# Optimization experiments

Hardware: AMD Instinct MI355X
Metric: run time of the kernel (lower is better)

Reference implementation:

```python
import jax, jax.numpy as jnp
import numpy as np

N = 100000   # total nodes (batched molecular graph)
E = 200000   # total edges
G = 5000     # number of graphs
NF = 16      # num_node_features
EF = 8       # num_edge_features
LD = 64      # latent_dim
EPS = 1e-5   # batch-norm eps (PyG BatchNorm default)


def setup_inputs() -> dict:
    key = jax.random.key(0)
    ks = jax.random.split(key, 20)
    s = 0.1  # weight scale
    return {
        'x': jax.random.normal(ks[0], (N, NF), dtype=jnp.float32),
        'edge_index': jax.random.randint(ks[1], (2, E), 0, N, dtype=jnp.int32),
        'edge_attr': jax.random.normal(ks[2], (E, EF), dtype=jnp.float32),
        'batch': jnp.sort(jax.random.randint(ks[3], (N,), 0, G, dtype=jnp.int32)),
        # ECC layer 1 (in=16 -> out=32)
        'We1': jax.random.normal(ks[4], (NF * 32, EF), dtype=jnp.float32) * s,
        'b1': jnp.zeros((32,), dtype=jnp.float32),
        'Wr1': jax.random.normal(ks[5], (32, NF), dtype=jnp.float32) * s,
        'g1': jnp.ones((32,), dtype=jnp.float32),
        'be1': jnp.zeros((32,), dtype=jnp.float32),
        # ECC layer 2 (in=32 -> out=64)
        'We2': jax.random.normal(ks[6], (32 * 64, EF), dtype=jnp.float32) * s,
        'b2': jnp.zeros((64,), dtype=jnp.float32),
        'Wr2': jax.random.normal(ks[7], (64, 32), dtype=jnp.float32) * s,
        'g2': jnp.ones((64,), dtype=jnp.float32),
        'be2': jnp.zeros((64,), dtype=jnp.float32),
        # dense tail
        'Wf1': jax.random.normal(ks[8], (128, 64), dtype=jnp.float32) * s,
        'bf1': jnp.zeros((128,), dtype=jnp.float32),
        'Wf2': jax.random.normal(ks[9], (2 * LD, 128), dtype=jnp.float32) * s,
        'bf2': jnp.zeros((2 * LD,), dtype=jnp.float32),
    }


def _ecc(x, src, dst, edge_attr, We, b, Wr, out_c):
    # theta: per-edge [out_c, in_c] filter matrices from edge features
    in_c = x.shape[1]
    theta = (edge_attr @ We.T).reshape(-1, out_c, in_c)       # [E, out, in]
    deg = jnp.zeros((x.shape[0],), x.dtype).at[src].add(1.0)   # degree over edge_index[0]
    norm = jnp.where(deg > 0, 1.0 / deg, 0.0)                  # [N]
    msg = jnp.einsum('eoi,ei->eo', theta, x[src]) * norm[src, None]  # [E, out]
    agg = jnp.zeros((x.shape[0], out_c), x.dtype).at[dst].add(msg)   # scatter-add
    return agg + b + x @ Wr.T


def _bn(x, g, be):
    # training-mode batch norm over the node dimension
    mu = jnp.mean(x, axis=0)
    var = jnp.mean((x - mu) ** 2, axis=0)
    return (x - mu) * jax.lax.rsqrt(var + EPS) * g + be


def reference(x, edge_index, edge_attr, batch,
              We1, b1, Wr1, g1, be1,
              We2, b2, Wr2, g2, be2,
              Wf1, bf1, Wf2, bf2):
    src, dst = edge_index[0], edge_index[1]
    h = _ecc(x, src, dst, edge_attr, We1, b1, Wr1, 32)
    h = jax.nn.relu(_bn(h, g1, be1))
    h = _ecc(h, src, dst, edge_attr, We2, b2, Wr2, 64)
    h = jax.nn.relu(_bn(h, g2, be2))
    # global mean pool over graphs
    sums = jax.ops.segment_sum(h, batch, num_segments=G)
    cnts = jax.ops.segment_sum(jnp.ones((h.shape[0],), h.dtype), batch, num_segments=G)
    pooled = sums / jnp.maximum(cnts, 1.0)[:, None]            # [G, 64]
    h = jax.nn.relu(pooled @ Wf1.T + bf1)
    out = h @ Wf2.T + bf2                                      # [G, 2*LD]
    mu_z = out[:, :LD]
    log_sigma = out[:, LD:]
    return mu_z, log_sigma
```

## Files before the change

### kernel.cpp

```cpp
#include <hip/hip_runtime.h>

#define NN 100000
#define NE 200000
#define NG 5000
#define EPSI 1e-5f
#define NBLK 98

using short8 = __attribute__((ext_vector_type(8))) short;
using f32x4  = __attribute__((ext_vector_type(4))) float;

static __device__ inline short bfbits(float f) {
    __bf16 b = (__bf16)f;
    return __builtin_bit_cast(short, b);
}
static __device__ inline float bf2f(short s) {
    unsigned u = ((unsigned)(unsigned short)s) << 16;
    return __builtin_bit_cast(float, u);
}

constexpr long FZ_NRM  = 0;
constexpr long FZ_STAT = NN;
constexpr long FZ_DCNT = NN + 512;
constexpr long ZN_FAST = 2L * NN + 512;
constexpr long O_OFFS  = ZN_FAST;
constexpr long O_CURS  = O_OFFS + NN;
constexpr long O_PERM  = O_CURS + NN;
constexpr long O_GLO   = O_PERM + NE;
constexpr long O_BSUM  = O_GLO + NG + 1;
constexpr long O_POOL  = ((O_BSUM + 256 + 3) & ~3L);
constexpr long O_H1    = O_POOL + 64L * NG;
constexpr long O_OUT2  = O_H1 + 32L * NN;
constexpr long O_MSG2  = O_OUT2 + 64L * NN;
constexpr long O_H1B   = O_MSG2 + 32L * NE;
constexpr long TOTAL_FAST = O_MSG2 + 64L * NE;

constexpr long B_NORM = 0;
constexpr long B_AGG1 = NN;
constexpr long B_AGG2 = B_AGG1 + 32L * NN;
constexpr long B_GSUM = B_AGG2 + 64L * NN;
constexpr long B_GCNT = B_GSUM + 64L * NG;
constexpr long B_STAT = B_GCNT + NG;
constexpr long ZERO_FB = B_STAT + 512;


__global__ void k_norm(float* __restrict__ deg) {
    int n = blockIdx.x * blockDim.x + threadIdx.x;
    if (n < NN) { float d = deg[n]; deg[n] = d > 0.f ? 1.f / d : 0.f; }
}

template <int CI, int COLS, bool HB>
__global__ void __launch_bounds__(64 * (COLS / 16))
k_edge_lds(const int* __restrict__ ei, const float* __restrict__ ea,
           const void* __restrict__ hraw, const float* __restrict__ W,
           const float* __restrict__ nrm, unsigned short* __restrict__ msg)
{
    constexpr int KS = CI / 4;
    constexpr int TILES = COLS / 16;
    constexpr int BT = 64 * TILES;
    constexpr int HP  = 20;
    constexpr int HPB = 36;
    constexpr int NGRP = NE / 32;
    constexpr int TPR = BT / 32;
    constexpr int EPT = 256 / BT;
    constexpr int HBYTES = HB ? (32 * HPB * 2) : (32 * HP * 4);

    const int tid  = threadIdx.x;
    const int lane = tid & 63;
    const int wid  = tid >> 6;
    const int c = lane & 15;
    const int q = lane >> 4;

    short8 bfr[KS];
    {
        const float* wrow = W + (wid * 16 + c) * (CI * 8) + q * 8;
        #pragma unroll
        for (int kk = 0; kk < KS; ++kk) {
            const float* p = wrow + kk * 32;
            #pragma unroll
            for (int j = 0; j < 8; ++j) bfr[kk][j] = bfbits(p[j]);
        }
    }

    __shared__ __align__(16) unsigned char h_raw[2][HBYTES];
    __shared__ float ea_lds[2][32 * 9];

    const int hrow = tid / TPR;
    const int hj0  = (tid % TPR) * 4;
    const int erow = tid >> 3;
    const int ef   = tid & 7;

    auto writebuf = [&](int buf, float4 hv, ushort4 hu, float ev0, float ev1) {
        if constexpr (HB) {
            *reinterpret_cast<ushort4*>(
                (unsigned short*)h_raw[buf] + hrow * HPB + hj0) = hu;
        } else {
            *reinterpret_cast<float4*>(
                (float*)h_raw[buf] + hrow * HP + hj0) = hv;
        }
        ea_lds[buf][erow * 9 + ef] = ev0;
        if constexpr (EPT == 2) ea_lds[buf][(erow + 16) * 9 + ef] = ev1;
    };

    auto compute = [&](int buf, long e0) {
        #pragma unroll
        for (int et = 0; et < 2; ++et) {
            const int r = et * 16 + c;
            float ev[8];
            #pragma unroll
            for (int j = 0; j < 8; ++j) ev[j] = ea_lds[buf][r * 9 + j];
            f32x4 acc = {0.f, 0.f, 0.f, 0.f};
            #pragma unroll
            for (int kk = 0; kk < KS; ++kk) {
                float hv;
                if constexpr (HB)
                    hv = bf2f((short)((const unsigned short*)h_raw[buf])[r * HPB + kk * 4 + q]);
                else
                    hv = ((const float*)h_raw[buf])[r * HP + kk * 4 + q];
                short8 afr;
                #pragma unroll
                for (int j = 0; j < 8; ++j) afr[j] = bfbits(hv * ev[j]);
                acc = __builtin_amdgcn_mfma_f32_16x16x32_bf16(afr, bfr[kk], acc, 0, 0, 0);
            }
            #pragma unroll
            for (int t = 0; t < 4; ++t) {
                msg[(e0 + et * 16 + q * 4 + t) * COLS + wid * 16 + c] =
                    (unsigned short)bfbits(acc[t]);
            }
        }
    };

    const int GD = gridDim.x;
    int g = blockIdx.x;
    if (g >= NGRP) return;

    int sh_c = ei[(long)g * 32 + hrow];
    int se0_c = ei[(long)g * 32 + erow];
    int se1_c = 0;
    if constexpr (EPT == 2) se1_c = ei[(long)g * 32 + erow + 16];
    int sh_n = 0, se0_n = 0, se1_n = 0;
    {
        int gn0 = g + GD;
        if (gn0 < NGRP) {
            sh_n = ei[(long)gn0 * 32 + hrow];
            se0_n = ei[(long)gn0 * 32 + erow];
            if constexpr (EPT == 2) se1_n = ei[(long)gn0 * 32 + erow + 16];
        }
    }
    float4 hv4 = {0.f, 0.f, 0.f, 0.f};
    ushort4 hu4 = {0, 0, 0, 0};
    float ev0 = 0.f, ev1 = 0.f;
    {
        if constexpr (HB)
            hu4 = *reinterpret_cast<const ushort4*>(
                (const unsigned short*)hraw + (long)sh_c * CI + hj0);
        else
            hv4 = *reinterpret_cast<const float4*>(
                (const float*)hraw + (long)sh_c * CI + hj0);
        ev0 = ea[((long)g * 32 + erow) * 8 + ef] * nrm[se0_c];
        if constexpr (EPT == 2)
            ev1 = ea[((long)g * 32 + erow + 16) * 8 + ef] * nrm[se1_c];
    }
    writebuf(0, hv4, hu4, ev0, ev1);
    __syncthreads();

    int p = 0;
    for (;;) {
        int gn = g + GD;
        bool more = (gn < NGRP);
        int gnn = gn + GD;
        int sh_f = 0, se0_f = 0, se1_f = 0;
        if (gnn < NGRP) {
            sh_f = ei[(long)gnn * 32 + hrow];
            se0_f = ei[(long)gnn * 32 + erow];
            if constexpr (EPT == 2) se1_f = ei[(long)gnn * 32 + erow + 16];
        }
        if (more) {
            if constexpr (HB)
                hu4 = *reinterpret_cast<const ushort4*>(
                    (const unsigned short*)hraw + (long)sh_n * CI + hj0);
            else
                hv4 = *reinterpret_cast<const float4*>(
                    (const float*)hraw + (long)sh_n * CI + hj0);
            ev0 = ea[((long)gn * 32 + erow) * 8 + ef] * nrm[se0_n];
            if constexpr (EPT == 2)
                ev1 = ea[((long)gn * 32 + erow + 16) * 8 + ef] * nrm[se1_n];
        }
        compute(p, (long)g * 32);
        if (!more) break;
        writebuf(p ^ 1, hv4, hu4, ev0, ev1);
        __syncthreads();
        sh_n = sh_f; se0_n = se0_f; se1_n = se1_f;
        g = gn; p ^= 1;
    }
}

template <int KS, int COLS>
__global__ void __launch_bounds__(256) k_edge_mfma_at(
    const int* __restrict__ ei, const float* __restrict__ ea,
    const float* __restrict__ h, const float* __restrict__ W,
    const float* __restrict__ nrm, float* __restrict__ outp)
{
    constexpr int TILES = COLS / 16;
    constexpr int CI = KS * 4;
    const int lane = threadIdx.x & 63;
    const int wid  = threadIdx.x >> 6;
    const int c = lane & 15;
    const int q = lane >> 4;
    const int gw = blockIdx.x * 4 + wid;
    const int ntile = gw % TILES;
    const int grp   = gw / TILES;
    if (grp >= NE / 16) return;
    short8 bfr[KS];
    {
        const float* wrow = W + (ntile * 16 + c) * (KS * 32) + q * 8;
        #pragma unroll
        for (int kk = 0; kk < KS; ++kk) {
            const float* p = wrow + kk * 32;
            #pragma unroll
            for (int j = 0; j < 8; ++j) bfr[kk][j] = bfbits(p[j]);
        }
    }
    const long e0 = (long)grp * 16;
    const long e  = e0 + c;
    const int  s  = ei[e];
    const float nv = nrm[s];
    float ev[8];
    {
        const float* p = ea + e * 8;
        #pragma unroll
        for (int j = 0; j < 8; ++j) ev[j] = p[j];
    }
    float hv[KS];
    {
        const float* hp = h + (long)s * CI + q;
        #pragma unroll
        for (int kk = 0; kk < KS; ++kk) hv[kk] = hp[kk * 4] * nv;
    }
    f32x4 acc = {0.f, 0.f, 0.f, 0.f};
    #pragma unroll
    for (int kk = 0; kk < KS; ++kk) {
        short8 afr;
        #pragma unroll
        for (int j = 0; j < 8; ++j) afr[j] = bfbits(hv[kk] * ev[j]);
        acc = __builtin_amdgcn_mfma_f32_16x16x32_bf16(afr, bfr[kk], acc, 0, 0, 0);
    }
    #pragma unroll
    for (int t = 0; t < 4; ++t) {
        int m = q * 4 + t;
        int d = ei[NE + e0 + m];
        atomicAdd(&outp[(long)d * COLS + ntile * 16 + c], acc[t]);
    }
}

template <int C>
__global__ void k_colstats(const float* __restrict__ v, float* __restrict__ sum,
                           float* __restrict__ ssq) {
    constexpr int RPB = 256 / C;
    const int c = threadIdx.x % C;
    const int r = threadIdx.x / C;
    float s = 0.f, q = 0.f;
    for (int n = blockIdx.x * RPB + r; n < NN; n += gridDim.x * RPB) {
        float val = v[(long)n * C + c];
        s += val; q += val * val;
    }
    __shared__ float ls[256], lq[256];
    ls[threadIdx.x] = s; lq[threadIdx.x] = q;
    __syncthreads();
    if (threadIdx.x < C) {
        float ts = 0.f, tq = 0.f;
        #pragma unroll
        for (int k = 0; k < RPB; ++k) { ts += ls[c + k * C]; tq += lq[c + k * C]; }
        atomicAdd(&sum[c], ts);
        atomicAdd(&ssq[c], tq);
    }
}

__global__ void k_fin(int C, const float* __restrict__ sum, const float* __restrict__ ssq,
                      const float* __restrict__ g, const float* __restrict__ be,
                      float* __restrict__ scale, float* __restrict__ shift) {
    int c = threadIdx.x;
    if (c < C) {
        float mu  = sum[c] / (float)NN;
        float var = ssq[c] / (float)NN - mu * mu;
        float rs  = rsqrtf(var + EPSI);
        float sc  = rs * g[c];
        scale[c] = sc;
        shift[c] = be[c] - mu * sc;
    }
}

__global__ void k_bnrelu32(const float* __restrict__ in, const float* __restrict__ scale,
                           const float* __restrict__ shift, float* __restrict__ outp) {
    long t = (long)blockIdx.x * blockDim.x + threadIdx.x;
    if (t < 32L * NN) {
        int c = (int)(t & 31);
        float v = in[t] * scale[c] + shift[c];
        outp[t] = v > 0.f ? v : 0.f;
    }
}

__global__ void __launch_bounds__(256) k_h1b(
    const float* __restrict__ h1, const float* __restrict__ scale,
    const float* __restrict__ shift, unsigned short* __restrict__ h1b)
{
    long t = (long)blockIdx.x * 256 + threadIdx.x;
    long base = t * 8;
    if (base >= 32L * NN) return;
    int c0 = (int)(base & 31);
    short8 outv;
    const float* p = h1 + base;
    #pragma unroll
    for (int j = 0; j < 8; ++j) {
        float v = fmaxf(fmaf(p[j], scale[c0 + j], shift[c0 + j]), 0.f);
        outv[j] = bfbits(v);
    }
    *reinterpret_cast<short8*>(h1b + base) = outv;
}

template <int CO>
__global__ void __launch_bounds__(256) k_msum(
    const unsigned short* __restrict__ msg, const int* __restrict__ offs,
    const int* __restrict__ dcnt, const int* __restrict__ perm,
    float* __restrict__ aggout)
{
    constexpr int CPN = CO / 4;
    long t = (long)blockIdx.x * 256 + threadIdx.x;
    long n = t / CPN;
    int chunk = (int)(t % CPN);
    if (n >= NN) return;
    int lo = offs[n], ct = dcnt[n];
    f32x4 a = {0.f, 0.f, 0.f, 0.f}, b = {0.f, 0.f, 0.f, 0.f};
    int j = 0;
    for (; j + 1 < ct; j += 2) {
        int e0p = perm[lo + j];
        int e1p = perm[lo + j + 1];
        ushort4 u0 = *reinterpret_cast<const ushort4*>(msg + (long)e0p * CO + chunk * 4);
        ushort4 u1 = *reinterpret_cast<const ushort4*>(msg + (long)e1p * CO + chunk * 4);
        a.x += bf2f((short)u0.x); a.y += bf2f((short)u0.y);
        a.z += bf2f((short)u0.z); a.w += bf2f((short)u0.w);
        b.x += bf2f((short)u1.x); b.y += bf2f((short)u1.y);
        b.z += bf2f((short)u1.z); b.w += bf2f((short)u1.w);
    }
    if (j < ct) {
        int e0p = perm[lo + j];
        ushort4 u0 = *reinterpret_cast<const ushort4*>(msg + (long)e0p * CO + chunk * 4);
        a.x += bf2f((short)u0.x); a.y += bf2f((short)u0.y);
        a.z += bf2f((short)u0.z); a.w += bf2f((short)u0.w);
    }
    a += b;
    *reinterpret_cast<f32x4*>(aggout + n * CO + chunk * 4) = a;
}

template <int CI, int CO, bool XB>
__global__ void __launch_bounds__(256) k_root(
    const void* __restrict__ Xraw, const float* __restrict__ W,
    const float* __restrict__ bias, float* __restrict__ Y,
    float* __restrict__ sum, float* __restrict__ ssq)
{
    constexpr int TILES = CO / 16;
    constexpr int MT = NN / 16;
    constexpr int MTPB = 4 / TILES;
    const int lane = threadIdx.x & 63;
    const int wid  = threadIdx.x >> 6;
    const int c = lane & 15;
    const int q = lane >> 4;
    const int ntile = (TILES == 4) ? wid : (wid & (TILES - 1));
    const int mtoff = (TILES == 4) ? 0 : (wid >> 1);
    const int o = ntile * 16 + c;
    const bool kvalid = (q * 8) < CI;

    short8 bhi = {0,0,0,0,0,0,0,0}, blo = {0,0,0,0,0,0,0,0};
    if (kvalid) {
        const float* wrow = W + (long)o * CI + q * 8;
        #pragma unroll
        for (int j = 0; j < 8; ++j) {
            float v = wrow[j];
            short h = bfbits(v);
            bhi[j] = h;
            blo[j] = bfbits(v - bf2f(h));
        }
    }
    const float bv = bias[o];
    float s_acc = 0.f, q_acc = 0.f;

    for (int mt = blockIdx.x * MTPB + mtoff; mt < MT; mt += gridDim.x * MTPB) {
        f32x4 acc = {0.f, 0.f, 0.f, 0.f};
        if constexpr (XB) {
            short8 ahi = {0,0,0,0,0,0,0,0};
            if (kvalid)
                ahi = *reinterpret_cast<const short8*>(
                    (const unsigned short*)Xraw + (long)(mt * 16 + c) * CI + q * 8);
            acc = __builtin_amdgcn_mfma_f32_16x16x32_bf16(ahi, bhi, acc, 0, 0, 0);
        } else {
            short8 ahi = {0,0,0,0,0,0,0,0}, alo = {0,0,0,0,0,0,0,0};
            if (kvalid) {
                const float* xp = (const float*)Xraw + (long)(mt * 16 + c) * CI + q * 8;
                #pragma unroll
                for (int j = 0; j < 8; ++j) {
                    float v = xp[j];
                    short h = bfbits(v);
                    ahi[j] = h;
                    alo[j] = bfbits(v - bf2f(h));
                }
            }
            acc = __builtin_amdgcn_mfma_f32_16x16x32_bf16(ahi, bhi, acc, 0, 0, 0);
            acc = __builtin_amdgcn_mfma_f32_16x16x32_bf16(ahi, blo, acc, 0, 0, 0);
            acc = __builtin_amdgcn_mfma_f32_16x16x32_bf16(alo, bhi, acc, 0, 0, 0);
        }
        #pragma unroll
        for (int t4 = 0; t4 < 4; ++t4) {
            long r = (long)mt * 16 + q * 4 + t4;
            long idx = r * CO + o;
            float v = Y[idx] + acc[t4] + bv;
            Y[idx] = v;
            s_acc += v;
            q_acc = fmaf(v, v, q_acc);
        }
    }

    __shared__ float ls[256], lq[256];
    ls[threadIdx.x] = s_acc; lq[threadIdx.x] = q_acc;
    __syncthreads();
    if (threadIdx.x < CO) {
        int ch = threadIdx.x;
        int bw = ch >> 4;
        int cc = ch & 15;
        float ts = 0.f, tq = 0.f;
        if (TILES == 4) {
            #pragma unroll
            for (int q2 = 0; q2 < 4; ++q2) {
                ts += ls[bw * 64 + q2 * 16 + cc];
                tq += lq[bw * 64 + q2 * 16 + cc];
            }
        } else {
            #pragma unroll
            for (int w2 = 0; w2 < 2; ++w2) {
                int w = bw + w2 * 2;
                #pragma unroll
                for (int q2 = 0; q2 < 4; ++q2) {
                    ts += ls[w * 64 + q2 * 16 + cc];
                    tq += lq[w * 64 + q2 * 16 + cc];
                }
            }
        }
        atomicAdd(&sum[ch], ts);
        atomicAdd(&ssq[ch], tq);
    }
}

template <int K, int NO, bool RELU, bool SPLITOUT>
__global__ void __launch_bounds__(256) k_fcmm(
    const float* __restrict__ X, const float* __restrict__ W,
    const float* __restrict__ bias, float* __restrict__ Y)
{
    constexpr int KS = K / 32;
    constexpr int TILES = NO / 16;
    constexpr int MT = (NG + 15) / 16;
    const int lane = threadIdx.x & 63;
    const int wid  = threadIdx.x >> 6;
    const int c = lane & 15;
    const int q = lane >> 4;
    const int gw = blockIdx.x * 4 + wid;
    const int ntile = gw % TILES;
    const int mt    = gw / TILES;
    if (mt >= MT) return;

    short8 bhi[KS], blo[KS];
    {
        const float* wrow = W + (ntile * 16 + c) * K + q * 8;
        #pragma unroll
        for (int kk = 0; kk < KS; ++kk) {
            const float* p = wrow + kk * 32;
            #pragma unroll
            for (int j = 0; j < 8; ++j) {
                float v = p[j];
                short h = bfbits(v);
                bhi[kk][j] = h;
                blo[kk][j] = bfbits(v - bf2f(h));
            }
        }
    }

    int arow = mt * 16 + c;
    if (arow > NG - 1) arow = NG - 1;
    const float* xp = X + (long)arow * K + q * 8;

    f32x4 acc = {0.f, 0.f, 0.f, 0.f};
    #pragma unroll
    for (int kk = 0; kk < KS; ++kk) {
        const float* p = xp + kk * 32;
        short8 ahi, alo;
        #pragma unroll
        for (int j = 0; j < 8; ++j) {
            float v = p[j];
            short h = bfbits(v);
            ahi[j] = h;
            alo[j] = bfbits(v - bf2f(h));
        }
        acc = __builtin_amdgcn_mfma_f32_16x16x32_bf16(ahi, bhi[kk], acc, 0, 0, 0);
        acc = __builtin_amdgcn_mfma_f32_16x16x32_bf16(ahi, blo[kk], acc, 0, 0, 0);
        acc = __builtin_amdgcn_mfma_f32_16x16x32_bf16(alo, bhi[kk], acc, 0, 0, 0);
    }

    const int o = ntile * 16 + c;
    const float bv = bias[o];
    #pragma unroll
    for (int t = 0; t < 4; ++t) {
        int r = mt * 16 + q * 4 + t;
        if (r < NG) {
            float v = acc[t] + bv;
            if (RELU) v = v > 0.f ? v : 0.f;
            if (SPLITOUT) {
                if (o < 64) Y[(long)r * 64 + o] = v;
                else        Y[(long)NG * 64 + (long)r * 64 + (o - 64)] = v;
            } else {
                Y[(long)r * NO + o] = v;
            }
        }
    }
}

__global__ void k_fc(const float* __restrict__ pooled,
                     const float* __restrict__ Wf1, const float* __restrict__ bf1,
                     const float* __restrict__ Wf2, const float* __restrict__ bf2,
                     float* __restrict__ outp) {
    const int lane = threadIdx.x & 63;
    int gw = (blockIdx.x * blockDim.x + threadIdx.x) >> 6;
    int nw = (gridDim.x * blockDim.x) >> 6;
    for (int g = gw; g < NG; g += nw) {
        float pl = pooled[(long)g * 64 + lane];
        float f1a = bf1[lane], f1b = bf1[lane + 64];
        const float* w1a = Wf1 + lane * 64;
        const float* w1b = Wf1 + (lane + 64) * 64;
        #pragma unroll 8
        for (int i = 0; i < 64; ++i) {
            float pv = __shfl(pl, i);
            f1a += pv * w1a[i];
            f1b += pv * w1b[i];
        }
        f1a = f1a > 0.f ? f1a : 0.f;
        f1b = f1b > 0.f ? f1b : 0.f;
        float oa = bf2[lane], ob = bf2[lane + 64];
        const float* w2a = Wf2 + lane * 128;
        const float* w2b = Wf2 + (lane + 64) * 128;
        #pragma unroll 8
        for (int i = 0; i < 64; ++i) {
            float va = __shfl(f1a, i);
            float vb = __shfl(f1b, i);
            oa += va * w2a[i] + vb * w2a[64 + i];
            ob += va * w2b[i] + vb * w2b[64 + i];
        }
        outp[(long)g * 64 + lane] = oa;
        outp[(long)NG * 64 + (long)g * 64 + lane] = ob;
    }
}


__global__ void k_degcnt(const int* __restrict__ ei, float* __restrict__ deg,
                         int* __restrict__ dcnt) {
    int e = blockIdx.x * blockDim.x + threadIdx.x;
    if (e < NE) {
        atomicAdd(&deg[ei[e]], 1.0f);
        atomicAdd(&dcnt[ei[NE + e]], 1);
    }
}

__global__ void k_scanA(const int* __restrict__ dcnt, int* __restrict__ offs,
                        int* __restrict__ bsum, float* __restrict__ deg) {
    int tid = threadIdx.x, b = blockIdx.x;
    int base = b * 1024 + tid * 4;
    int v[4]; int t = 0;
    #pragma unroll
    for (int k = 0; k < 4; ++k) { v[k] = (base + k < NN) ? dcnt[base + k] : 0; t += v[k]; }
    #pragma unroll
    for (int k = 0; k < 4; ++k) {
        int i = base + k;
        if (i < NN) { float d = deg[i]; deg[i] = d > 0.f ? 1.f / d : 0.f; }
    }
    __shared__ int s[256];
    s[tid] = t;
    __syncthreads();
    for (int d = 1; d < 256; d <<= 1) {
        int x = (tid >= d) ? s[tid - d] : 0;
        __syncthreads();
        s[tid] += x;
        __syncthreads();
    }
    int excl = s[tid] - t;
    int o = excl;
    #pragma unroll
    for (int k = 0; k < 4; ++k) {
        if (base + k < NN) offs[base + k] = o;
        o += v[k];
    }
    if (tid == 255) bsum[b] = s[255];
}

__global__ void k_scanB(int* __restrict__ bsum) {
    int tid = threadIdx.x;
    __shared__ int s[128];
    int val = (tid < NBLK) ? bsum[tid] : 0;
    s[tid] = val;
    __syncthreads();
    for (int d = 1; d < 128; d <<= 1) {
        int x = (tid >= d) ? s[tid - d] : 0;
        __syncthreads();
        s[tid] += x;
        __syncthreads();
    }
    bsum[tid] = s[tid] - val;
}

__global__ void k_scanC(int* __restrict__ offs, int* __restrict__ curs,
                        const int* __restrict__ bsum) {
    int tid = threadIdx.x, b = blockIdx.x;
    int base = b * 1024 + tid * 4;
    int add = bsum[b];
    #pragma unroll
    for (int k = 0; k < 4; ++k) {
        int i = base + k;
        if (i < NN) { int o = offs[i] + add; offs[i] = o; curs[i] = o; }
    }
}

__global__ void k_scatter(const int* __restrict__ ei, int* __restrict__ curs,
                          int* __restrict__ perm, const int* __restrict__ batch,
                          int* __restrict__ glo) {
    int e = blockIdx.x * blockDim.x + threadIdx.x;
    if (e < NE) {
        int d = ei[NE + e];
        int pos = atomicAdd(&curs[d], 1);
        perm[pos] = e;
    }
    if (e <= NG) {
        int lo = 0, hi = NN;
        while (lo < hi) { int m = (lo + hi) >> 1; if (batch[m] < e) lo = m + 1; else hi = m; }
        glo[e] = lo;
    }
}

__global__ void k_poolg(const float* __restrict__ out2, const int* __restrict__ glo,
                        const float* __restrict__ scale, const float* __restrict__ shift,
                        float* __restrict__ pooled) {
    const int lane = threadIdx.x & 63;
    int g = (blockIdx.x * blockDim.x + threadIdx.x) >> 6;
    if (g >= NG) return;
    int lo = glo[g], hi = glo[g + 1];
    float sc = scale[lane], sh = shift[lane];
    float acc = 0.f;
    for (int n = lo; n < hi; ++n) {
        float v = out2[(long)n * 64 + lane] * sc + sh;
        acc += v > 0.f ? v : 0.f;
    }
    float m = (float)(hi - lo);
    pooled[(long)g * 64 + lane] = acc / (m > 1.f ? m : 1.f);
}


__global__ void k_deg(const int* __restrict__ ei, float* __restrict__ deg) {
    int e = blockIdx.x * blockDim.x + threadIdx.x;
    if (e < NE) atomicAdd(&deg[ei[e]], 1.0f);
}

template <int CI, int CO>
__global__ void k_nodeadd(const float* __restrict__ xin, const float* __restrict__ Wr,
                          const float* __restrict__ b, float* __restrict__ outp) {
    constexpr int NPW = 64 / CO;
    const int lane = threadIdx.x & 63;
    const int c = lane % CO;
    const int sub = lane / CO;
    float w[CI];
    #pragma unroll
    for (int i = 0; i < CI; ++i) w[i] = Wr[c * CI + i];
    float bias = b[c];
    int gw = (blockIdx.x * blockDim.x + threadIdx.x) >> 6;
    int nw = (gridDim.x * blockDim.x) >> 6;
    for (int n0 = gw * NPW; n0 < NN; n0 += nw * NPW) {
        int n = n0 + sub;
        if (n < NN) {
            const float* xp = xin + (long)n * CI;
            float acc = outp[(long)n * CO + c] + bias;
            #pragma unroll
            for (int i = 0; i < CI; ++i) acc += xp[i] * w[i];
            outp[(long)n * CO + c] = acc;
        }
    }
}

__global__ void k_pool_at(const float* __restrict__ out2, const int* __restrict__ batch,
                          const float* __restrict__ scale, const float* __restrict__ shift,
                          float* __restrict__ gsum) {
    long t = (long)blockIdx.x * blockDim.x + threadIdx.x;
    int c = (int)(t & 63);
    long n0 = (t >> 6) * 4;
    if (n0 >= NN) return;
    float sc = scale[c], sh = shift[c];
    float acc = 0.f;
    int gprev = batch[n0];
    #pragma unroll
    for (int k = 0; k < 4; ++k) {
        long n = n0 + k;
        if (n >= NN) break;
        int g = batch[n];
        float v = out2[n * 64 + c] * sc + sh;
        v = v > 0.f ? v : 0.f;
        if (g != gprev) {
            atomicAdd(&gsum[(long)gprev * 64 + c], acc);
            acc = 0.f; gprev = g;
        }
        acc += v;
    }
    atomicAdd(&gsum[(long)gprev * 64 + c], acc);
}

__global__ void k_cnt(const int* __restrict__ batch, float* __restrict__ gcnt) {
    int n = blockIdx.x * blockDim.x + threadIdx.x;
    if (n < NN) atomicAdd(&gcnt[batch[n]], 1.0f);
}

__global__ void k_div(float* __restrict__ gsum, const float* __restrict__ gcnt) {
    long t = (long)blockIdx.x * blockDim.x + threadIdx.x;
    if (t < 64L * NG) {
        float cnt = gcnt[t >> 6];
        gsum[t] = gsum[t] / (cnt > 1.f ? cnt : 1.f);
    }
}


extern "C" void kernel_launch(void* const* d_in, const int* in_sizes, int n_in,
                              void* d_out, int out_size, void* d_ws, size_t ws_size,
                              hipStream_t stream) {
    const float* x   = (const float*)d_in[0];
    const int*   ei  = (const int*)d_in[1];
    const float* ea  = (const float*)d_in[2];
    const int*   bat = (const int*)d_in[3];
    const float* We1 = (const float*)d_in[4];
    const float* b1  = (const float*)d_in[5];
    const float* Wr1 = (const float*)d_in[6];
    const float* g1  = (const float*)d_in[7];
    const float* be1 = (const float*)d_in[8];
    const float* We2 = (const float*)d_in[9];
    const float* b2  = (const float*)d_in[10];
    const float* Wr2 = (const float*)d_in[11];
    const float* g2  = (const float*)d_in[12];
    const float* be2 = (const float*)d_in[13];
    const float* Wf1 = (const float*)d_in[14];
    const float* bf1 = (const float*)d_in[15];
    const float* Wf2 = (const float*)d_in[16];
    const float* bf2 = (const float*)d_in[17];
    float* out = (float*)d_out;
    float* ws  = (float*)d_ws;
    int*   wsi = (int*)d_ws;

    if (ws_size >= (size_t)TOTAL_FAST * sizeof(float)) {
        float* nrm    = ws + FZ_NRM;
        float* st     = ws + FZ_STAT;
        int*   dcnt   = wsi + FZ_DCNT;
        int*   offs   = wsi + O_OFFS;
        int*   curs   = wsi + O_CURS;
        int*   perm   = wsi + O_PERM;
        int*   glo    = wsi + O_GLO;
        int*   bsum   = wsi + O_BSUM;
        float* pooled = ws + O_POOL;
        float* h1     = ws + O_H1;
        float* out2   = ws + O_OUT2;
        unsigned short* msg1 = (unsigned short*)(ws + O_OUT2);
        unsigned short* msg2 = (unsigned short*)(ws + O_MSG2);
        unsigned short* h1b  = (unsigned short*)(ws + O_H1B);
        float* fc1out = ws + O_MSG2;
        float* sums1 = st;        float* ssq1 = st + 32;
        float* sums2 = st + 64;   float* ssq2 = st + 128;
        float* sc1   = st + 192;  float* sh1  = st + 224;
        float* sc2   = st + 256;  float* sh2  = st + 320;

        hipMemsetAsync(d_ws, 0, (size_t)ZN_FAST * sizeof(float), stream);

        k_degcnt<<<(NE + 255) / 256, 256, 0, stream>>>(ei, nrm, dcnt);
        k_scanA<<<NBLK, 256, 0, stream>>>(dcnt, offs, bsum, nrm);
        k_scanB<<<1, 128, 0, stream>>>(bsum);
        k_scanC<<<NBLK, 256, 0, stream>>>(offs, curs, bsum);
        k_scatter<<<(NE + 255) / 256, 256, 0, stream>>>(ei, curs, perm, bat, glo);

        k_edge_lds<16, 32, false><<<2048, 128, 0, stream>>>(
            ei, ea, x, We1, nrm, msg1);
        k_msum<32><<<3125, 256, 0, stream>>>(msg1, offs, dcnt, perm, h1);
        k_root<16, 32, false><<<512, 256, 0, stream>>>(
            x, Wr1, b1, h1, sums1, ssq1);
        k_fin<<<1, 64, 0, stream>>>(32, sums1, ssq1, g1, be1, sc1, sh1);
        k_h1b<<<(int)((32L * NN / 8 + 255) / 256), 256, 0, stream>>>(h1, sc1, sh1, h1b);

        k_edge_lds<32, 64, true><<<2048, 256, 0, stream>>>(
            ei, ea, h1b, We2, nrm, msg2);
        k_msum<64><<<6250, 256, 0, stream>>>(msg2, offs, dcnt, perm, out2);
        k_root<32, 64, true><<<512, 256, 0, stream>>>(
            h1b, Wr2, b2, out2, sums2, ssq2);
        k_fin<<<1, 64, 0, stream>>>(64, sums2, ssq2, g2, be2, sc2, sh2);

        k_poolg<<<1250, 256, 0, stream>>>(out2, glo, sc2, sh2, pooled);

        {
            constexpr int MT = (NG + 15) / 16;
            k_fcmm<64, 128, true,  false><<<(MT * 8 + 3) / 4, 256, 0, stream>>>(pooled, Wf1, bf1, fc1out);
            k_fcmm<128, 128, false, true><<<(MT * 8 + 3) / 4, 256, 0, stream>>>(fc1out, Wf2, bf2, out);
        }
    } else {
        float* nrm   = ws + B_NORM;
        float* agg1  = ws + B_AGG1;
        float* agg2  = ws + B_AGG2;
        float* gsum  = ws + B_GSUM;
        float* gcnt  = ws + B_GCNT;
        float* st    = ws + B_STAT;
        float* sums1 = st;        float* ssq1 = st + 32;
        float* sums2 = st + 64;   float* ssq2 = st + 128;
        float* sc1   = st + 192;  float* sh1  = st + 224;
        float* sc2   = st + 256;  float* sh2  = st + 320;

        hipMemsetAsync(d_ws, 0, (size_t)ZERO_FB * sizeof(float), stream);

        k_deg<<<(NE + 255) / 256, 256, 0, stream>>>(ei, nrm);
        k_norm<<<(NN + 255) / 256, 256, 0, stream>>>(nrm);

        k_edge_mfma_at<4, 32><<<6250, 256, 0, stream>>>(ei, ea, x, We1, nrm, agg1);
        k_nodeadd<16, 32><<<1024, 256, 0, stream>>>(x, Wr1, b1, agg1);
        k_colstats<32><<<1024, 256, 0, stream>>>(agg1, sums1, ssq1);
        k_fin<<<1, 64, 0, stream>>>(32, sums1, ssq1, g1, be1, sc1, sh1);
        k_bnrelu32<<<(int)((32L * NN + 255) / 256), 256, 0, stream>>>(agg1, sc1, sh1, agg1);

        k_edge_mfma_at<8, 64><<<12500, 256, 0, stream>>>(ei, ea, agg1, We2, nrm, agg2);
        k_nodeadd<32, 64><<<1024, 256, 0, stream>>>(agg1, Wr2, b2, agg2);
        k_colstats<64><<<1024, 256, 0, stream>>>(agg2, sums2, ssq2);
        k_fin<<<1, 64, 0, stream>>>(64, sums2, ssq2, g2, be2, sc2, sh2);

        k_pool_at<<<6250, 256, 0, stream>>>(agg2, bat, sc2, sh2, gsum);
        k_cnt<<<(NN + 255) / 256, 256, 0, stream>>>(bat, gcnt);
        k_div<<<(int)((64L * NG + 255) / 256), 256, 0, stream>>>(gsum, gcnt);
        k_fc<<<1250, 256, 0, stream>>>(gsum, Wf1, bf1, Wf2, bf2, out);
    }
}
```

Before: 189.8 us.

## Fuse CSR message gather-sum into root MFMA kernel with BN statistics

Removes the separate k_msum kernels and performs the per-node CSR gather of bf16 messages inside the root-transform MFMA kernel, so each output element is written once instead of written by msum then read-modified-written by root. This eliminates two launches and a full read/write pass over the aggregate buffer per layer. In exchange, each lane gathers scalar bf16 values (2-byte loads) rather than 8-byte vector chunks, so gather coalescing is worse. Grid sizes are raised to supply more parallelism for the gather.

```diff
diff --git a/kernel.cpp b/kernel.cpp
--- a/kernel.cpp
+++ b/kernel.cpp
@@ -317,45 +317,13 @@
     *reinterpret_cast<short8*>(h1b + base) = outv;
 }
 
-template <int CO>
-__global__ void __launch_bounds__(256) k_msum(
+template <int CI, int CO, bool XB>
+__global__ void __launch_bounds__(256) k_rootm(
+    const void* __restrict__ Xraw, const float* __restrict__ W,
+    const float* __restrict__ bias,
     const unsigned short* __restrict__ msg, const int* __restrict__ offs,
     const int* __restrict__ dcnt, const int* __restrict__ perm,
-    float* __restrict__ aggout)
-{
-    constexpr int CPN = CO / 4;
-    long t = (long)blockIdx.x * 256 + threadIdx.x;
-    long n = t / CPN;
-    int chunk = (int)(t % CPN);
-    if (n >= NN) return;
-    int lo = offs[n], ct = dcnt[n];
-    f32x4 a = {0.f, 0.f, 0.f, 0.f}, b = {0.f, 0.f, 0.f, 0.f};
-    int j = 0;
-    for (; j + 1 < ct; j += 2) {
-        int e0p = perm[lo + j];
-        int e1p = perm[lo + j + 1];
-        ushort4 u0 = *reinterpret_cast<const ushort4*>(msg + (long)e0p * CO + chunk * 4);
-        ushort4 u1 = *reinterpret_cast<const ushort4*>(msg + (long)e1p * CO + chunk * 4);
-        a.x += bf2f((short)u0.x); a.y += bf2f((short)u0.y);
-        a.z += bf2f((short)u0.z); a.w += bf2f((short)u0.w);
-        b.x += bf2f((short)u1.x); b.y += bf2f((short)u1.y);
-        b.z += bf2f((short)u1.z); b.w += bf2f((short)u1.w);
-    }
-    if (j < ct) {
-        int e0p = perm[lo + j];
-        ushort4 u0 = *reinterpret_cast<const ushort4*>(msg + (long)e0p * CO + chunk * 4);
-        a.x += bf2f((short)u0.x); a.y += bf2f((short)u0.y);
-        a.z += bf2f((short)u0.z); a.w += bf2f((short)u0.w);
-    }
-    a += b;
-    *reinterpret_cast<f32x4*>(aggout + n * CO + chunk * 4) = a;
-}
-
-template <int CI, int CO, bool XB>
-__global__ void __launch_bounds__(256) k_root(
-    const void* __restrict__ Xraw, const float* __restrict__ W,
-    const float* __restrict__ bias, float* __restrict__ Y,
-    float* __restrict__ sum, float* __restrict__ ssq)
+    float* __restrict__ Y, float* __restrict__ sum, float* __restrict__ ssq)
 {
     constexpr int TILES = CO / 16;
     constexpr int MT = NN / 16;
@@ -384,6 +352,13 @@
     float s_acc = 0.f, q_acc = 0.f;
 
     for (int mt = blockIdx.x * MTPB + mtoff; mt < MT; mt += gridDim.x * MTPB) {
+        int lo[4], ct[4];
+        #pragma unroll
+        for (int t4 = 0; t4 < 4; ++t4) {
+            int r = mt * 16 + q * 4 + t4;
+            lo[t4] = offs[r];
+            ct[t4] = dcnt[r];
+        }
         f32x4 acc = {0.f, 0.f, 0.f, 0.f};
         if constexpr (XB) {
             short8 ahi = {0,0,0,0,0,0,0,0};
@@ -407,12 +382,28 @@
             acc = __builtin_amdgcn_mfma_f32_16x16x32_bf16(ahi, blo, acc, 0, 0, 0);
             acc = __builtin_amdgcn_mfma_f32_16x16x32_bf16(alo, bhi, acc, 0, 0, 0);
         }
+        float ms[4];
+        #pragma unroll
+        for (int t4 = 0; t4 < 4; ++t4) {
+            float a = 0.f, b = 0.f;
+            int j = 0;
+            for (; j + 1 < ct[t4]; j += 2) {
+                int ep0 = perm[lo[t4] + j];
+                int ep1 = perm[lo[t4] + j + 1];
+                a += bf2f((short)msg[(long)ep0 * CO + o]);
+                b += bf2f((short)msg[(long)ep1 * CO + o]);
+            }
+            if (j < ct[t4]) {
+                int ep0 = perm[lo[t4] + j];
+                a += bf2f((short)msg[(long)ep0 * CO + o]);
+            }
+            ms[t4] = a + b;
+        }
         #pragma unroll
         for (int t4 = 0; t4 < 4; ++t4) {
             long r = (long)mt * 16 + q * 4 + t4;
-            long idx = r * CO + o;
-            float v = Y[idx] + acc[t4] + bv;
-            Y[idx] = v;
+            float v = acc[t4] + ms[t4] + bv;
+            Y[r * CO + o] = v;
             s_acc += v;
             q_acc = fmaf(v, v, q_acc);
         }
@@ -783,17 +774,15 @@
 
         k_edge_lds<16, 32, false><<<2048, 128, 0, stream>>>(
             ei, ea, x, We1, nrm, msg1);
-        k_msum<32><<<3125, 256, 0, stream>>>(msg1, offs, dcnt, perm, h1);
-        k_root<16, 32, false><<<512, 256, 0, stream>>>(
-            x, Wr1, b1, h1, sums1, ssq1);
+        k_rootm<16, 32, false><<<1024, 256, 0, stream>>>(
+            x, Wr1, b1, msg1, offs, dcnt, perm, h1, sums1, ssq1);
         k_fin<<<1, 64, 0, stream>>>(32, sums1, ssq1, g1, be1, sc1, sh1);
         k_h1b<<<(int)((32L * NN / 8 + 255) / 256), 256, 0, stream>>>(h1, sc1, sh1, h1b);
 
         k_edge_lds<32, 64, true><<<2048, 256, 0, stream>>>(
             ei, ea, h1b, We2, nrm, msg2);
-        k_msum<64><<<6250, 256, 0, stream>>>(msg2, offs, dcnt, perm, out2);
-        k_root<32, 64, true><<<512, 256, 0, stream>>>(
-            h1b, Wr2, b2, out2, sums2, ssq2);
+        k_rootm<32, 64, true><<<1568, 256, 0, stream>>>(
+            h1b, Wr2, b2, msg2, offs, dcnt, perm, out2, sums2, ssq2);
         k_fin<<<1, 64, 0, stream>>>(64, sums2, ssq2, g2, be2, sc2, sh2);
 
         k_poolg<<<1250, 256, 0, stream>>>(out2, glo, sc2, sh2, pooled);
```

New measurement: 229.2 us. 20.7% more time.

## Fold BN finalize, scan-B and FC layers into neighboring kernels

Applied to the files above, without the earlier changes.

Removes four small launches. The two batch-norm finalize kernels are folded into their consumers (k_h1b and k_poolg), which now recompute scale and shift per block. The single-block scan of block sums is replaced by a per-block reduction inside k_scanC. The two FC matmul kernels are merged into one kernel that keeps the 16x128 intermediate in LDS. This cuts launch overhead and serialization gaps, at the cost of redundant per-block work and a fused kernel with fewer blocks.

```diff
diff --git a/kernel.cpp b/kernel.cpp
--- a/kernel.cpp
+++ b/kernel.cpp
@@ -300,9 +300,21 @@
 }
 
 __global__ void __launch_bounds__(256) k_h1b(
-    const float* __restrict__ h1, const float* __restrict__ scale,
-    const float* __restrict__ shift, unsigned short* __restrict__ h1b)
+    const float* __restrict__ h1, const float* __restrict__ sums,
+    const float* __restrict__ ssq, const float* __restrict__ g,
+    const float* __restrict__ be, unsigned short* __restrict__ h1b)
 {
+    __shared__ float sc[32], sh[32];
+    if (threadIdx.x < 32) {
+        int c = threadIdx.x;
+        float mu  = sums[c] / (float)NN;
+        float var = ssq[c] / (float)NN - mu * mu;
+        float rs  = rsqrtf(var + EPSI);
+        float s   = rs * g[c];
+        sc[c] = s;
+        sh[c] = be[c] - mu * s;
+    }
+    __syncthreads();
     long t = (long)blockIdx.x * 256 + threadIdx.x;
     long base = t * 8;
     if (base >= 32L * NN) return;
@@ -311,7 +323,7 @@
     const float* p = h1 + base;
     #pragma unroll
     for (int j = 0; j < 8; ++j) {
-        float v = fmaxf(fmaf(p[j], scale[c0 + j], shift[c0 + j]), 0.f);
+        float v = fmaxf(fmaf(p[j], sc[c0 + j], sh[c0 + j]), 0.f);
         outv[j] = bfbits(v);
     }
     *reinterpret_cast<short8*>(h1b + base) = outv;
@@ -448,29 +460,54 @@
     }
 }
 
-template <int K, int NO, bool RELU, bool SPLITOUT>
-__global__ void __launch_bounds__(256) k_fcmm(
-    const float* __restrict__ X, const float* __restrict__ W,
-    const float* __restrict__ bias, float* __restrict__ Y)
+__global__ void k_poolg(const float* __restrict__ out2, const int* __restrict__ glo,
+                        const float* __restrict__ sums, const float* __restrict__ ssq,
+                        const float* __restrict__ g2, const float* __restrict__ be2,
+                        float* __restrict__ pooled) {
+    const int lane = threadIdx.x & 63;
+    int g = (blockIdx.x * blockDim.x + threadIdx.x) >> 6;
+    if (g >= NG) return;
+    float mu  = sums[lane] / (float)NN;
+    float var = ssq[lane] / (float)NN - mu * mu;
+    float rs  = rsqrtf(var + EPSI);
+    float sc  = rs * g2[lane];
+    float sh  = be2[lane] - mu * sc;
+    int lo = glo[g], hi = glo[g + 1];
+    float acc = 0.f;
+    for (int n = lo; n < hi; ++n) {
+        float v = out2[(long)n * 64 + lane] * sc + sh;
+        acc += v > 0.f ? v : 0.f;
+    }
+    float m = (float)(hi - lo);
+    pooled[(long)g * 64 + lane] = acc / (m > 1.f ? m : 1.f);
+}
+
+__global__ void __launch_bounds__(256) k_fcfused(
+    const float* __restrict__ pooled,
+    const float* __restrict__ Wf1, const float* __restrict__ bf1,
+    const float* __restrict__ Wf2, const float* __restrict__ bf2,
+    float* __restrict__ outp)
 {
-    constexpr int KS = K / 32;
-    constexpr int TILES = NO / 16;
     constexpr int MT = (NG + 15) / 16;
     const int lane = threadIdx.x & 63;
     const int wid  = threadIdx.x >> 6;
     const int c = lane & 15;
     const int q = lane >> 4;
-    const int gw = blockIdx.x * 4 + wid;
-    const int ntile = gw % TILES;
-    const int mt    = gw / TILES;
+    const int mt = blockIdx.x;
     if (mt >= MT) return;
 
-    short8 bhi[KS], blo[KS];
-    {
-        const float* wrow = W + (ntile * 16 + c) * K + q * 8;
-        #pragma unroll
-        for (int kk = 0; kk < KS; ++kk) {
-            const float* p = wrow + kk * 32;
+    __shared__ float f1[16][132];
+
+    int arow = mt * 16 + c;
+    if (arow > NG - 1) arow = NG - 1;
+
+    #pragma unroll
+    for (int nt2 = 0; nt2 < 2; ++nt2) {
+        const int o = (wid * 2 + nt2) * 16 + c;
+        short8 bhi[2], blo[2];
+        #pragma unroll
+        for (int kk = 0; kk < 2; ++kk) {
+            const float* p = Wf1 + (long)o * 64 + kk * 32 + q * 8;
             #pragma unroll
             for (int j = 0; j < 8; ++j) {
                 float v = p[j];
@@ -479,42 +516,72 @@
                 blo[kk][j] = bfbits(v - bf2f(h));
             }
         }
-    }
-
-    int arow = mt * 16 + c;
-    if (arow > NG - 1) arow = NG - 1;
-    const float* xp = X + (long)arow * K + q * 8;
-
-    f32x4 acc = {0.f, 0.f, 0.f, 0.f};
-    #pragma unroll
-    for (int kk = 0; kk < KS; ++kk) {
-        const float* p = xp + kk * 32;
-        short8 ahi, alo;
-        #pragma unroll
-        for (int j = 0; j < 8; ++j) {
-            float v = p[j];
-            short h = bfbits(v);
-            ahi[j] = h;
-            alo[j] = bfbits(v - bf2f(h));
-        }
-        acc = __builtin_amdgcn_mfma_f32_16x16x32_bf16(ahi, bhi[kk], acc, 0, 0, 0);
-        acc = __builtin_amdgcn_mfma_f32_16x16x32_bf16(ahi, blo[kk], acc, 0, 0, 0);
-        acc = __builtin_amdgcn_mfma_f32_16x16x32_bf16(alo, bhi[kk], acc, 0, 0, 0);
-    }
-
-    const int o = ntile * 16 + c;
-    const float bv = bias[o];
-    #pragma unroll
-    for (int t = 0; t < 4; ++t) {
-        int r = mt * 16 + q * 4 + t;
-        if (r < NG) {
+        const float* xp = pooled + (long)arow * 64 + q * 8;
+        f32x4 acc = {0.f, 0.f, 0.f, 0.f};
+        #pragma unroll
+        for (int kk = 0; kk < 2; ++kk) {
+            const float* p = xp + kk * 32;
+            short8 ahi, alo;
+            #pragma unroll
+            for (int j = 0; j < 8; ++j) {
+                float v = p[j];
+                short h = bfbits(v);
+                ahi[j] = h;
+                alo[j] = bfbits(v - bf2f(h));
+            }
+            acc = __builtin_amdgcn_mfma_f32_16x16x32_bf16(ahi, bhi[kk], acc, 0, 0, 0);
+            acc = __builtin_amdgcn_mfma_f32_16x16x32_bf16(ahi, blo[kk], acc, 0, 0, 0);
+            acc = __builtin_amdgcn_mfma_f32_16x16x32_bf16(alo, bhi[kk], acc, 0, 0, 0);
+        }
+        const float bv = bf1[o];
+        #pragma unroll
+        for (int t = 0; t < 4; ++t) {
             float v = acc[t] + bv;
-            if (RELU) v = v > 0.f ? v : 0.f;
-            if (SPLITOUT) {
-                if (o < 64) Y[(long)r * 64 + o] = v;
-                else        Y[(long)NG * 64 + (long)r * 64 + (o - 64)] = v;
-            } else {
-                Y[(long)r * NO + o] = v;
+            f1[q * 4 + t][o] = v > 0.f ? v : 0.f;
+        }
+    }
+    __syncthreads();
+
+    #pragma unroll
+    for (int nt2 = 0; nt2 < 2; ++nt2) {
+        const int o = (wid * 2 + nt2) * 16 + c;
+        f32x4 acc = {0.f, 0.f, 0.f, 0.f};
+        #pragma unroll
+        for (int kk = 0; kk < 4; ++kk) {
+            short8 bhi, blo;
+            {
+                const float* p = Wf2 + (long)o * 128 + kk * 32 + q * 8;
+                #pragma unroll
+                for (int j = 0; j < 8; ++j) {
+                    float v = p[j];
+                    short h = bfbits(v);
+                    bhi[j] = h;
+                    blo[j] = bfbits(v - bf2f(h));
+                }
+            }
+            short8 ahi, alo;
+            {
+                const float* p = &f1[c][kk * 32 + q * 8];
+                #pragma unroll
+                for (int j = 0; j < 8; ++j) {
+                    float v = p[j];
+                    short h = bfbits(v);
+                    ahi[j] = h;
+                    alo[j] = bfbits(v - bf2f(h));
+                }
+            }
+            acc = __builtin_amdgcn_mfma_f32_16x16x32_bf16(ahi, bhi, acc, 0, 0, 0);
+            acc = __builtin_amdgcn_mfma_f32_16x16x32_bf16(ahi, blo, acc, 0, 0, 0);
+            acc = __builtin_amdgcn_mfma_f32_16x16x32_bf16(alo, bhi, acc, 0, 0, 0);
+        }
+        const float bv = bf2[o];
+        #pragma unroll
+        for (int t = 0; t < 4; ++t) {
+            int r = mt * 16 + q * 4 + t;
+            if (r < NG) {
+                float v = acc[t] + bv;
+                if (o < 64) outp[(long)r * 64 + o] = v;
+                else        outp[(long)NG * 64 + (long)r * 64 + (o - 64)] = v;
             }
         }
     }
@@ -596,26 +663,18 @@
     if (tid == 255) bsum[b] = s[255];
 }
 
-__global__ void k_scanB(int* __restrict__ bsum) {
-    int tid = threadIdx.x;
-    __shared__ int s[128];
-    int val = (tid < NBLK) ? bsum[tid] : 0;
-    s[tid] = val;
-    __syncthreads();
-    for (int d = 1; d < 128; d <<= 1) {
-        int x = (tid >= d) ? s[tid - d] : 0;
-        __syncthreads();
-        s[tid] += x;
-        __syncthreads();
-    }
-    bsum[tid] = s[tid] - val;
-}
-
 __global__ void k_scanC(int* __restrict__ offs, int* __restrict__ curs,
                         const int* __restrict__ bsum) {
     int tid = threadIdx.x, b = blockIdx.x;
+    __shared__ int sacc[128];
+    if (tid < 128) sacc[tid] = (tid < b) ? bsum[tid] : 0;
+    __syncthreads();
+    for (int d = 64; d > 0; d >>= 1) {
+        if (tid < d) sacc[tid] += sacc[tid + d];
+        __syncthreads();
+    }
+    int add = sacc[0];
     int base = b * 1024 + tid * 4;
-    int add = bsum[b];
     #pragma unroll
     for (int k = 0; k < 4; ++k) {
         int i = base + k;
@@ -637,23 +696,6 @@
         while (lo < hi) { int m = (lo + hi) >> 1; if (batch[m] < e) lo = m + 1; else hi = m; }
         glo[e] = lo;
     }
-}
-
-__global__ void k_poolg(const float* __restrict__ out2, const int* __restrict__ glo,
-                        const float* __restrict__ scale, const float* __restrict__ shift,
-                        float* __restrict__ pooled) {
-    const int lane = threadIdx.x & 63;
-    int g = (blockIdx.x * blockDim.x + threadIdx.x) >> 6;
-    if (g >= NG) return;
-    int lo = glo[g], hi = glo[g + 1];
-    float sc = scale[lane], sh = shift[lane];
-    float acc = 0.f;
-    for (int n = lo; n < hi; ++n) {
-        float v = out2[(long)n * 64 + lane] * sc + sh;
-        acc += v > 0.f ? v : 0.f;
-    }
-    float m = (float)(hi - lo);
-    pooled[(long)g * 64 + lane] = acc / (m > 1.f ? m : 1.f);
 }
 
 
@@ -767,17 +809,13 @@
         unsigned short* msg1 = (unsigned short*)(ws + O_OUT2);
         unsigned short* msg2 = (unsigned short*)(ws + O_MSG2);
         unsigned short* h1b  = (unsigned short*)(ws + O_H1B);
-        float* fc1out = ws + O_MSG2;
         float* sums1 = st;        float* ssq1 = st + 32;
         float* sums2 = st + 64;   float* ssq2 = st + 128;
-        float* sc1   = st + 192;  float* sh1  = st + 224;
-        float* sc2   = st + 256;  float* sh2  = st + 320;
 
         hipMemsetAsync(d_ws, 0, (size_t)ZN_FAST * sizeof(float), stream);
 
         k_degcnt<<<(NE + 255) / 256, 256, 0, stream>>>(ei, nrm, dcnt);
         k_scanA<<<NBLK, 256, 0, stream>>>(dcnt, offs, bsum, nrm);
-        k_scanB<<<1, 128, 0, stream>>>(bsum);
         k_scanC<<<NBLK, 256, 0, stream>>>(offs, curs, bsum);
         k_scatter<<<(NE + 255) / 256, 256, 0, stream>>>(ei, curs, perm, bat, glo);
 
@@ -786,23 +824,17 @@
         k_msum<32><<<3125, 256, 0, stream>>>(msg1, offs, dcnt, perm, h1);
         k_root<16, 32, false><<<512, 256, 0, stream>>>(
             x, Wr1, b1, h1, sums1, ssq1);
-        k_fin<<<1, 64, 0, stream>>>(32, sums1, ssq1, g1, be1, sc1, sh1);
-        k_h1b<<<(int)((32L * NN / 8 + 255) / 256), 256, 0, stream>>>(h1, sc1, sh1, h1b);
+        k_h1b<<<(int)((32L * NN / 8 + 255) / 256), 256, 0, stream>>>(
+            h1, sums1, ssq1, g1, be1, h1b);
 
         k_edge_lds<32, 64, true><<<2048, 256, 0, stream>>>(
             ei, ea, h1b, We2, nrm, msg2);
         k_msum<64><<<6250, 256, 0, stream>>>(msg2, offs, dcnt, perm, out2);
         k_root<32, 64, true><<<512, 256, 0, stream>>>(
             h1b, Wr2, b2, out2, sums2, ssq2);
-        k_fin<<<1, 64, 0, stream>>>(64, sums2, ssq2, g2, be2, sc2, sh2);
-
-        k_poolg<<<1250, 256, 0, stream>>>(out2, glo, sc2, sh2, pooled);
-
-        {
-            constexpr int MT = (NG + 15) / 16;
-            k_fcmm<64, 128, true,  false><<<(MT * 8 + 3) / 4, 256, 0, stream>>>(pooled, Wf1, bf1, fc1out);
-            k_fcmm<128, 128, false, true><<<(MT * 8 + 3) / 4, 256, 0, stream>>>(fc1out, Wf2, bf2, out);
-        }
+
+        k_poolg<<<1250, 256, 0, stream>>>(out2, glo, sums2, ssq2, g2, be2, pooled);
+        k_fcfused<<<(NG + 15) / 16, 256, 0, stream>>>(pooled, Wf1, bf1, Wf2, bf2, out);
     } else {
         float* nrm   = ws + B_NORM;
         float* agg1  = ws + B_AGG1;
```

New measurement: 184.4 us. -2.9%, faster.
